# Optimization experiments

Measured on AMD Instinct MI355X. Metric: run time of the kernel, lower is better.

Reference implementation:

```python
import jax, jax.numpy as jnp
import numpy as np

N_SRC = 50000
N_TGT = 50000
E = 320000
D = 256          # feature dim == hidden_channels
H = 256
OUT = 16
L = 2
P_DROP = 0.1
NEG_SLOPE = 0.01  # F.leaky_relu default


def _seg_mean(x, src_idx, dst_idx, n_dst):
    # gather source features along edges, mean-aggregate per destination (PyG SAGE default aggr='mean')
    msgs = x[src_idx]                                            # [E, D]
    s = jax.ops.segment_sum(msgs, dst_idx, num_segments=n_dst)   # [n_dst, D]
    cnt = jax.ops.segment_sum(jnp.ones((dst_idx.shape[0],), x.dtype), dst_idx, num_segments=n_dst)
    return s / jnp.maximum(cnt, 1.0)[:, None]


def _dropout(x, p, key):
    keep = jax.random.bernoulli(key, 1.0 - p, x.shape)
    return jnp.where(keep, x / (1.0 - p), jnp.zeros((), x.dtype))


def setup_inputs() -> dict:
    key = jax.random.key(0)
    ks = jax.random.split(key, 16)
    sc_in = 1.0 / np.sqrt(D)
    sc_h = 1.0 / np.sqrt(H)
    inp = {
        'x_source': jax.random.normal(ks[0], (N_SRC, D), jnp.float32),
        'x_target': jax.random.normal(ks[1], (N_TGT, D), jnp.float32),
        'ei_st': jax.random.randint(ks[2], (2, E), 0, N_SRC, jnp.int32),  # row0: source idx, row1: target idx
        'ei_ts': jax.random.randint(ks[3], (2, E), 0, N_TGT, jnp.int32),  # row0: target idx, row1: source idx
        # SAGEConv params per layer per relation; lin_l has bias, lin_r does not (PyG)
        'Wl_st': jax.random.normal(ks[4], (L, D, H), jnp.float32) * sc_in,
        'Wr_st': jax.random.normal(ks[5], (L, D, H), jnp.float32) * sc_in,
        'b_st': jnp.zeros((L, H), jnp.float32),
        'Wl_ts': jax.random.normal(ks[6], (L, D, H), jnp.float32) * sc_in,
        'Wr_ts': jax.random.normal(ks[7], (L, D, H), jnp.float32) * sc_in,
        'b_ts': jnp.zeros((L, H), jnp.float32),
        'Wout': jax.random.normal(ks[8], (H, OUT), jnp.float32) * sc_h,
        'bout': jnp.zeros((OUT,), jnp.float32),
    }
    return inp


def reference(x_source, x_target, ei_st, ei_ts, Wl_st, Wr_st, b_st, Wl_ts, Wr_ts, b_ts, Wout, bout):
    drop_key = jax.random.key(42)
    x_s, x_t = x_source, x_target
    for l in range(L):
        # relation ('source','edge','target'): messages source -> target
        m_t = _seg_mean(x_s, ei_st[0], ei_st[1], N_TGT)
        new_t = m_t @ Wl_st[l] + b_st[l] + x_t @ Wr_st[l]
        # relation ('target','rev_edge','source'): messages target -> source
        m_s = _seg_mean(x_t, ei_ts[0], ei_ts[1], N_SRC)
        new_s = m_s @ Wl_ts[l] + b_ts[l] + x_s @ Wr_ts[l]
        # leaky_relu + dropout (F.dropout default training=True)
        new_s = jnp.where(new_s >= 0, new_s, NEG_SLOPE * new_s)
        new_t = jnp.where(new_t >= 0, new_t, NEG_SLOPE * new_t)
        x_s = _dropout(new_s, P_DROP, jax.random.fold_in(drop_key, 2 * l))
        x_t = _dropout(new_t, P_DROP, jax.random.fold_in(drop_key, 2 * l + 1))
    return x_s @ Wout + bout  # [N_SRC, OUT]
```

## Files before the change

### kernel.cpp

```cpp
#include <hip/hip_runtime.h>
#include <stdint.h>

#define NSRC 50000
#define NTGT 50000
#define NE   320000
#define DIN  256
#define HID  256
#define DOUT 16

#define GBM 64
#define GBLK ((NSRC + GBM - 1) / GBM)
#define MASK_DW_PER (GBLK * 512)

typedef __attribute__((ext_vector_type(8))) short bf16x8;
typedef __attribute__((ext_vector_type(4))) float f32x4;
typedef __attribute__((ext_vector_type(4))) uint u32x4;

__device__ inline ushort f2b(float f) {
  uint32_t u = __float_as_uint(f);
  return (ushort)((u + 0x7FFFu + ((u >> 16) & 1u)) >> 16);
}
__device__ inline float b2f(ushort h) { return __uint_as_float(((uint32_t)h) << 16); }

typedef __attribute__((address_space(3))) uint32_t lds_u32_t;
typedef const __attribute__((address_space(1))) uint32_t glb_u32_t;
__device__ __forceinline__ void ld_lds16(const ushort* g, ushort* lds) {
  __builtin_amdgcn_global_load_lds((glb_u32_t*)g, (lds_u32_t*)lds, 16, 0, 0);
}

__host__ __device__ constexpr uint64_t tf2x32(uint32_t k0, uint32_t k1,
                                              uint32_t x0, uint32_t x1) {
  uint32_t ks2 = k0 ^ k1 ^ 0x1BD11BDAu;
  x0 += k0; x1 += k1;
#define TF_ROT(x, r) (((x) << (r)) | ((x) >> (32 - (r))))
#define TF_RND(r) { x0 += x1; x1 = TF_ROT(x1, r) ^ x0; }
  TF_RND(13) TF_RND(15) TF_RND(26) TF_RND(6)
  x0 += k1;  x1 += ks2 + 1u;
  TF_RND(17) TF_RND(29) TF_RND(16) TF_RND(24)
  x0 += ks2; x1 += k0 + 2u;
  TF_RND(13) TF_RND(15) TF_RND(26) TF_RND(6)
  x0 += k0;  x1 += k1 + 3u;
  TF_RND(17) TF_RND(29) TF_RND(16) TF_RND(24)
  x0 += k1;  x1 += ks2 + 4u;
  TF_RND(13) TF_RND(15) TF_RND(26) TF_RND(6)
  x0 += ks2; x1 += k0 + 5u;
#undef TF_RND
#undef TF_ROT
  return (uint64_t(x0) << 32) | uint64_t(x1);
}

constexpr uint64_t FOLD[4] = {
  tf2x32(0u, 42u, 0u, 0u),
  tf2x32(0u, 42u, 0u, 1u),
  tf2x32(0u, 42u, 0u, 2u),
  tf2x32(0u, 42u, 0u, 3u),
};

__device__ __forceinline__ void mask_word(uint32_t* __restrict__ masks, int d) {
  int g = d / MASK_DW_PER;
  int w = d - g * MASK_DW_PER;
  int gt = w >> 1, half = w & 1;
  int gblk = gt >> 8, gtid = gt & 255;
  int wave = gtid >> 6, lane = gtid & 63;
  int q = lane >> 4, r = lane & 15;
  uint64_t fk = (g == 0) ? FOLD[1] : (g == 1 ? FOLD[0] : FOLD[2]);
  uint32_t kk0 = (uint32_t)(fk >> 32), kk1 = (uint32_t)fk;
  int mbase = gblk * GBM;
  uint32_t mword = 0;
#pragma unroll
  for (int bb = 0; bb < 32; ++bb) {
    int s = half * 32 + bb;
    int si = s >> 4, se = (s >> 2) & 3, sj = s & 3;
    uint32_t rowg = (uint32_t)(mbase + si * 16 + q * 4 + se);
    uint32_t colg = (uint32_t)(wave * 64 + sj * 16 + r);
    uint64_t rr = tf2x32(kk0, kk1, 0u, rowg * 256u + colg);
    uint32_t bits = (uint32_t)(rr >> 32) ^ (uint32_t)rr;
    mword |= (((bits >> 9) < 7549747u) ? 1u : 0u) << bb;
  }
  masks[d] = mword;
}

#define NB_CVT  25000
#define NB_W    96
#define NB_HIST 2500
#define PREP_T  (NB_CVT + NB_W + NB_HIST)

struct PrepArgs {
  const float *xs, *xt;
  ushort *oxs, *oxt;
  const float* wsrc[6];
  ushort* wdst[6];
  const int *ei_a, *ei_b;
  int *cur_a, *cur_b;
};

__global__ __launch_bounds__(256) void prep_kernel(PrepArgs p) {
  __shared__ ushort tile[64][65];
  int blk = (int)(((long long)blockIdx.x * 97) % PREP_T);
  int tid = threadIdx.x;
  if (blk < NB_CVT) {
    const float* in = blk < (NB_CVT / 2) ? p.xs : p.xt;
    ushort* out = blk < (NB_CVT / 2) ? p.oxs : p.oxt;
    int i = (blk % (NB_CVT / 2)) * 256 + tid;
    float4 v = ((const float4*)in)[i];
    ushort4 o;
    o.x = f2b(v.x); o.y = f2b(v.y); o.z = f2b(v.z); o.w = f2b(v.w);
    ((ushort4*)out)[i] = o;
    return;
  }
  blk -= NB_CVT;
  if (blk < NB_W) {
    const float* W = p.wsrc[blk >> 4];
    ushort* Wt = p.wdst[blk >> 4];
    int ktile = (blk >> 2) & 3, ntile = blk & 3;
#pragma unroll
    for (int rep = 0; rep < 16; ++rep) {
      int lin = rep * 256 + tid;
      int kk = lin >> 6, nn = lin & 63;
      tile[nn][kk] = f2b(W[(size_t)(ktile * 64 + kk) * 256 + ntile * 64 + nn]);
    }
    __syncthreads();
#pragma unroll
    for (int rep = 0; rep < 16; ++rep) {
      int lin = rep * 256 + tid;
      int nn = lin >> 6, kk = lin & 63;
      Wt[(size_t)(ntile * 64 + nn) * 256 + ktile * 64 + kk] = tile[nn][kk];
    }
    return;
  }
  blk -= NB_W;
  const int* ei = blk < (NB_HIST / 2) ? p.ei_a : p.ei_b;
  int* cur = blk < (NB_HIST / 2) ? p.cur_a : p.cur_b;
  int e = (blk % (NB_HIST / 2)) * 256 + tid;
  if (e < NE) atomicAdd(cur + ei[NE + e], 1);
}

#define SB 1024
__global__ __launch_bounds__(SB) void scan_partial(const int* __restrict__ cur_a,
                                                   const int* __restrict__ cur_b,
                                                   int* __restrict__ bsum,
                                                   int n, int nbPer) {
  __shared__ int red[SB];
  int b = blockIdx.x;
  const int* cnt = b < nbPer ? cur_a : cur_b;
  int i = (b % nbPer) * SB + threadIdx.x;
  red[threadIdx.x] = (i < n) ? cnt[i] : 0;
  __syncthreads();
  for (int d = SB / 2; d > 0; d >>= 1) {
    if (threadIdx.x < d) red[threadIdx.x] += red[threadIdx.x + d];
    __syncthreads();
  }
  if (threadIdx.x == 0) bsum[b] = red[0];
}

__global__ __launch_bounds__(128) void scan_base(int* __restrict__ bsum, int nbPer) {
  __shared__ int buf[2][64];
  int half = threadIdx.x >> 6;
  int t = threadIdx.x & 63;
  buf[half][t] = (t < nbPer) ? bsum[half * nbPer + t] : 0;
  __syncthreads();
  for (int d = 1; d < 64; d <<= 1) {
    int v = (t >= d) ? buf[half][t - d] : 0;
    __syncthreads();
    buf[half][t] += v;
    __syncthreads();
  }
  if (t < nbPer) bsum[half * nbPer + t] = (t == 0) ? 0 : buf[half][t - 1];
}

__global__ __launch_bounds__(SB) void scan_final(int* __restrict__ cur_a,
                                                 int* __restrict__ cur_b,
                                                 int* __restrict__ offs_a,
                                                 int* __restrict__ offs_b,
                                                 const int* __restrict__ bsum,
                                                 int n, int nbPer) {
  __shared__ int part[SB];
  int b = blockIdx.x;
  bool first = b < nbPer;
  int* cur = first ? cur_a : cur_b;
  int* offs = first ? offs_a : offs_b;
  int i = (b % nbPer) * SB + threadIdx.x;
  int v = (i < n) ? cur[i] : 0;
  part[threadIdx.x] = v;
  __syncthreads();
  for (int d = 1; d < SB; d <<= 1) {
    int tv = (threadIdx.x >= d) ? part[threadIdx.x - d] : 0;
    __syncthreads();
    part[threadIdx.x] += tv;
    __syncthreads();
  }
  int excl = part[threadIdx.x] - v + bsum[b];
  if (i < n) {
    offs[i] = excl;
    cur[i] = 0;
  }
  if (i == n - 1) offs[n] = excl + v;
}

__global__ __launch_bounds__(256) void csr_fill2(const int* __restrict__ ei_a,
                                                 const int* __restrict__ ei_b,
                                                 const int* __restrict__ offs_a,
                                                 const int* __restrict__ offs_b,
                                                 int* __restrict__ cur_a,
                                                 int* __restrict__ cur_b,
                                                 int* __restrict__ adj_a,
                                                 int* __restrict__ adj_b,
                                                 int nE, int nbPer) {
  int blk = blockIdx.x;
  bool first = blk < nbPer;
  const int* ei = first ? ei_a : ei_b;
  const int* offs = first ? offs_a : offs_b;
  int* cur = first ? cur_a : cur_b;
  int* adj = first ? adj_a : adj_b;
  int e = (blk % nbPer) * 256 + threadIdx.x;
  if (e >= nE) return;
  int dst = ei[nE + e];
  int pos = atomicAdd(cur + dst, 1);
  adj[offs[dst] + pos] = ei[e];
}

#define ACC8(vv)                                                              \
  {                                                                           \
    const ushort* u = (const ushort*)&vv;                                     \
    a0 += b2f(u[0]); a1 += b2f(u[1]); a2 += b2f(u[2]); a3 += b2f(u[3]);       \
    a4 += b2f(u[4]); a5 += b2f(u[5]); a6 += b2f(u[6]); a7 += b2f(u[7]);       \
  }

__device__ __forceinline__ void gather_row8(const ushort* __restrict__ x,
                                            const int* __restrict__ offs,
                                            const int* __restrict__ adj,
                                            ushort* __restrict__ m,
                                            int row, int lane) {
  int start = offs[row], end = offs[row + 1];
  float a0 = 0.f, a1 = 0.f, a2 = 0.f, a3 = 0.f;
  float a4 = 0.f, a5 = 0.f, a6 = 0.f, a7 = 0.f;
  const ushort* xb = x + lane * 8;
  int e = start;
  for (; e + 7 < end; e += 8) {
    int s0 = adj[e],     s1 = adj[e + 1], s2 = adj[e + 2], s3 = adj[e + 3];
    int s4 = adj[e + 4], s5 = adj[e + 5], s6 = adj[e + 6], s7 = adj[e + 7];
    u32x4 v0 = *(const u32x4*)(xb + (size_t)s0 * DIN);
    u32x4 v1 = *(const u32x4*)(xb + (size_t)s1 * DIN);
    u32x4 v2 = *(const u32x4*)(xb + (size_t)s2 * DIN);
    u32x4 v3 = *(const u32x4*)(xb + (size_t)s3 * DIN);
    u32x4 v4 = *(const u32x4*)(xb + (size_t)s4 * DIN);
    u32x4 v5 = *(const u32x4*)(xb + (size_t)s5 * DIN);
    u32x4 v6 = *(const u32x4*)(xb + (size_t)s6 * DIN);
    u32x4 v7 = *(const u32x4*)(xb + (size_t)s7 * DIN);
    ACC8(v0) ACC8(v1) ACC8(v2) ACC8(v3) ACC8(v4) ACC8(v5) ACC8(v6) ACC8(v7)
  }
  for (; e + 3 < end; e += 4) {
    int s0 = adj[e], s1 = adj[e + 1], s2 = adj[e + 2], s3 = adj[e + 3];
    u32x4 v0 = *(const u32x4*)(xb + (size_t)s0 * DIN);
    u32x4 v1 = *(const u32x4*)(xb + (size_t)s1 * DIN);
    u32x4 v2 = *(const u32x4*)(xb + (size_t)s2 * DIN);
    u32x4 v3 = *(const u32x4*)(xb + (size_t)s3 * DIN);
    ACC8(v0) ACC8(v1) ACC8(v2) ACC8(v3)
  }
  for (; e < end; ++e) {
    int s = adj[e];
    u32x4 v = *(const u32x4*)(xb + (size_t)s * DIN);
    ACC8(v)
  }
  float inv = 1.0f / fmaxf((float)(end - start), 1.0f);
  ushort o[8];
  o[0] = f2b(a0 * inv); o[1] = f2b(a1 * inv); o[2] = f2b(a2 * inv); o[3] = f2b(a3 * inv);
  o[4] = f2b(a4 * inv); o[5] = f2b(a5 * inv); o[6] = f2b(a6 * inv); o[7] = f2b(a7 * inv);
  *(u32x4*)(m + (size_t)row * DIN + lane * 8) = *(const u32x4*)o;
}

#define GG_GB 6250
#define G2_MASKB (2 * MASK_DW_PER / 256)
#define GM_T (GG_GB + G2_MASKB)

__global__ __launch_bounds__(256) void gather_mask_h(
    const ushort* __restrict__ x, const int* __restrict__ offs,
    const int* __restrict__ adj, ushort* __restrict__ m,
    uint32_t* __restrict__ masks, int nRows) {
  int blk = (int)(((long long)blockIdx.x * 97) % GM_T);
  int tid = threadIdx.x;
  if (blk >= GG_GB) {
    mask_word(masks, (blk - GG_GB) * 256 + tid);
    return;
  }
  int row = blk * 8 + (tid >> 5);
  if (row < nRows) gather_row8(x, offs, adj, m, row, tid & 31);
}

__device__ __forceinline__ void gemm_kloop(
    int bid, const ushort* __restrict__ A1, const ushort* __restrict__ A2,
    const ushort* __restrict__ W1t, const ushort* __restrict__ W2t,
    int M, ushort* sA, ushort* sB, f32x4 acc[4][4]) {
  const int tid = threadIdx.x;
  const int wave = tid >> 6, lane = tid & 63;
  const int q = lane >> 4, r = lane & 15;
  const int mbase = bid * GBM;

  const int arow = tid >> 2;
  const int akc = (tid & 3) * 8;
  const int agrow = min(mbase + arow, M - 1);
  const ushort* a1p = A1 + (size_t)agrow * DIN + akc;
  const ushort* a2p = A2 + (size_t)agrow * DIN + akc;
  const ushort* w1b = W1t + (size_t)arow * DIN + akc;
  const ushort* w2b = W2t + (size_t)arow * DIN + akc;
  ushort* ldsA0 = sA + wave * 512;
  ushort* ldsA1 = sA + 2048 + wave * 512;

#pragma unroll
  for (int t = 0; t < 8; ++t) {
    const int kt = t * 32;
    __syncthreads();
    ld_lds16(a1p + kt, ldsA0);
    ld_lds16(a2p + kt, ldsA1);
#pragma unroll
    for (int c = 0; c < 4; ++c) {
      ld_lds16(w1b + c * (64 * DIN) + kt, sB + c * 2048 + wave * 512);
      ld_lds16(w2b + c * (64 * DIN) + kt, sB + 8192 + c * 2048 + wave * 512);
    }
    __syncthreads();
#pragma unroll
    for (int ph = 0; ph < 2; ++ph) {
      bf16x8 af[4], bfr[4];
#pragma unroll
      for (int i = 0; i < 4; ++i)
        af[i] = *(const bf16x8*)&sA[ph * 2048 + (i * 16 + r) * 32 + q * 8];
#pragma unroll
      for (int j = 0; j < 4; ++j)
        bfr[j] = *(const bf16x8*)&sB[ph * 8192 + (wave * 64 + j * 16 + r) * 32 + q * 8];
#pragma unroll
      for (int i = 0; i < 4; ++i)
#pragma unroll
        for (int j = 0; j < 4; ++j)
          acc[i][j] = __builtin_amdgcn_mfma_f32_16x16x32_bf16(af[i], bfr[j],
                                                              acc[i][j], 0, 0, 0);
    }
  }
}

__device__ __forceinline__ void gemm_body(
    int bid, const ushort* __restrict__ A1, const ushort* __restrict__ A2,
    const ushort* __restrict__ W1t, const ushort* __restrict__ W2t,
    const float* __restrict__ bias, const uint2* __restrict__ mk,
    ushort* __restrict__ C, int M, ushort* sA, ushort* sB) {
  const int tid = threadIdx.x;
  const int wave = tid >> 6, lane = tid & 63;
  const int q = lane >> 4, r = lane & 15;
  const int mbase = bid * GBM;
  const uint2 km = mk[bid * 256 + tid];

  f32x4 acc[4][4] = {};
  gemm_kloop(bid, A1, A2, W1t, W2t, M, sA, sB, acc);

  float bj[4];
#pragma unroll
  for (int j = 0; j < 4; ++j) bj[j] = bias[wave * 64 + j * 16 + r];
#pragma unroll
  for (int i = 0; i < 4; ++i) {
#pragma unroll
    for (int e = 0; e < 4; ++e) {
      int rowg = mbase + i * 16 + q * 4 + e;
      if (rowg >= M) continue;
#pragma unroll
      for (int j = 0; j < 4; ++j) {
        const int s = i * 16 + e * 4 + j;
        int colg = wave * 64 + j * 16 + r;
        float v = acc[i][j][e] + bj[j];
        v = v >= 0.0f ? v : 0.01f * v;
        uint32_t keep = ((s < 32 ? km.x >> s : km.y >> (s - 32)) & 1u);
        v = keep ? v * (1.0f / 0.9f) : 0.0f;
        C[(size_t)rowg * HID + colg] = f2b(v);
      }
    }
  }
}

__global__ __launch_bounds__(256, 4) void gemm_dual_mfma(
    const ushort* __restrict__ A1, const ushort* __restrict__ A2,
    const ushort* __restrict__ W1t, const ushort* __restrict__ W2t,
    const float* __restrict__ bias, const uint2* __restrict__ mk,
    ushort* __restrict__ C, int M) {
  __shared__ ushort sA[2][GBM * 32];
  __shared__ ushort sB[2][HID * 32];
  gemm_body(blockIdx.x, A1, A2, W1t, W2t, bias, mk, C, M, &sA[0][0], &sB[0][0]);
}

#define GG_MASKB (MASK_DW_PER / 256)
#define G1_T (GBLK + GG_GB + GG_MASKB)

__global__ __launch_bounds__(256, 4) void gemm1_gather(
    const ushort* __restrict__ A1, const ushort* __restrict__ A2,
    const ushort* __restrict__ W1t, const ushort* __restrict__ W2t,
    const float* __restrict__ bias, const uint2* __restrict__ mk,
    ushort* __restrict__ C, int M,
    const ushort* __restrict__ gx, const int* __restrict__ goffs,
    const int* __restrict__ gadj, ushort* __restrict__ gm, int gRows,
    uint32_t* __restrict__ masks) {
  __shared__ ushort sA[2][GBM * 32];
  __shared__ ushort sB[2][HID * 32];
  int blk = (int)(((long long)blockIdx.x * 101) % G1_T);
  if (blk < GBLK) {
    gemm_body(blk, A1, A2, W1t, W2t, bias, mk, C, M, &sA[0][0], &sB[0][0]);
  } else if (blk < GBLK + GG_GB) {
    int row = (blk - GBLK) * 8 + (threadIdx.x >> 5);
    if (row < gRows) gather_row8(gx, goffs, gadj, gm, row, threadIdx.x & 31);
  } else {
    mask_word(masks,
              2 * MASK_DW_PER + (blk - GBLK - GG_GB) * 256 + (int)threadIdx.x);
  }
}

#define GG_T  (GBLK + GG_GB)

__global__ __launch_bounds__(256, 4) void gemm_gather(
    const ushort* __restrict__ A1, const ushort* __restrict__ A2,
    const ushort* __restrict__ W1t, const ushort* __restrict__ W2t,
    const float* __restrict__ bias, const uint2* __restrict__ mk,
    ushort* __restrict__ C, int M,
    const ushort* __restrict__ gx, const int* __restrict__ goffs,
    const int* __restrict__ gadj, ushort* __restrict__ gm, int gRows) {
  __shared__ ushort sA[2][GBM * 32];
  __shared__ ushort sB[2][HID * 32];
  int blk = (int)(((long long)blockIdx.x * 101) % GG_T);
  if (blk < GBLK) {
    gemm_body(blk, A1, A2, W1t, W2t, bias, mk, C, M, &sA[0][0], &sB[0][0]);
  } else {
    int row = (blk - GBLK) * 8 + (threadIdx.x >> 5);
    if (row < gRows) gather_row8(gx, goffs, gadj, gm, row, threadIdx.x & 31);
  }
}

__global__ __launch_bounds__(256) void out_gemm_h(const ushort* __restrict__ X,
                                                  const float* __restrict__ Wout,
                                                  const float* __restrict__ bout,
                                                  float* __restrict__ C, int M) {
  __shared__ float sW[DIN * DOUT];
  int tid = threadIdx.x;
#pragma unroll
  for (int i = 0; i < (DIN * DOUT) / 256; ++i) sW[i * 256 + tid] = Wout[i * 256 + tid];
  __syncthreads();
  int rr = tid >> 4, c = tid & 15;
  int row = blockIdx.x * 16 + rr;
  if (row >= M) return;
  float acc = bout[c];
  const ushort* xp = X + (size_t)row * DIN;
  for (int k = 0; k < DIN; k += 8) {
    uint4 u = *(const uint4*)(xp + k);
    const ushort* us = (const ushort*)&u;
#pragma unroll
    for (int t = 0; t < 8; ++t) acc += b2f(us[t]) * sW[(k + t) * DOUT + c];
  }
  C[(size_t)row * DOUT + c] = acc;
}

extern "C" void kernel_launch(void* const* d_in, const int* in_sizes, int n_in,
                              void* d_out, int out_size, void* d_ws, size_t ws_size,
                              hipStream_t stream) {
  const float* x_source = (const float*)d_in[0];
  const float* x_target = (const float*)d_in[1];
  const int* ei_st = (const int*)d_in[2];
  const int* ei_ts = (const int*)d_in[3];
  const float* Wl_st = (const float*)d_in[4];
  const float* Wr_st = (const float*)d_in[5];
  const float* b_st  = (const float*)d_in[6];
  const float* Wl_ts = (const float*)d_in[7];
  const float* Wr_ts = (const float*)d_in[8];
  const float* b_ts  = (const float*)d_in[9];
  const float* Wout  = (const float*)d_in[10];
  const float* bout  = (const float*)d_in[11];
  float* out = (float*)d_out;

  const size_t F = (size_t)NSRC * DIN;
  const size_t WM = (size_t)DIN * HID;
  const int nbScan = (NSRC + SB - 1) / SB;
  const size_t intCount = (NTGT + 1) + (NSRC + 1) + 2 * NE + NTGT + NSRC +
                          2 * nbScan + 3 * MASK_DW_PER;
  const size_t need = (5 * F + 6 * WM) * sizeof(ushort) + intCount * sizeof(int);
  if (ws_size < need) return;

  ushort* xs0h = (ushort*)d_ws;
  ushort* xt0h = xs0h + F;
  ushort* B0h  = xt0h + F;
  ushort* B1h  = B0h + F;
  ushort* B2h  = B1h + F;
  ushort* wt0  = B2h + F;
  ushort* wt1  = wt0 + WM;
  ushort* wt2  = wt1 + WM;
  ushort* wt3  = wt2 + WM;
  ushort* wt4  = wt3 + WM;
  ushort* wt5  = wt4 + WM;
  int* ip      = (int*)(wt5 + WM);
  int* offs_st = ip;
  int* offs_ts = offs_st + NTGT + 1;
  int* adj_st  = offs_ts + NSRC + 1;
  int* adj_ts  = adj_st + NE;
  int* cur_t   = adj_ts + NE;
  int* cur_s   = cur_t + NTGT;
  int* bsum    = cur_s + NSRC;
  uint32_t* masks = (uint32_t*)(bsum + 2 * nbScan);

  const int EB = (NE + 255) / 256;

  (void)hipMemsetAsync(cur_t, 0, (NTGT + NSRC) * sizeof(int), stream);
  PrepArgs pa;
  pa.xs = x_source; pa.xt = x_target; pa.oxs = xs0h; pa.oxt = xt0h;
  pa.wsrc[0] = Wl_st;      pa.wdst[0] = wt0;
  pa.wsrc[1] = Wr_st;      pa.wdst[1] = wt1;
  pa.wsrc[2] = Wl_ts;      pa.wdst[2] = wt2;
  pa.wsrc[3] = Wr_ts;      pa.wdst[3] = wt3;
  pa.wsrc[4] = Wl_ts + WM; pa.wdst[4] = wt4;
  pa.wsrc[5] = Wr_ts + WM; pa.wdst[5] = wt5;
  pa.ei_a = ei_st; pa.ei_b = ei_ts;
  pa.cur_a = cur_t; pa.cur_b = cur_s;
  prep_kernel<<<PREP_T, 256, 0, stream>>>(pa);

  scan_partial<<<2 * nbScan, SB, 0, stream>>>(cur_t, cur_s, bsum, NTGT, nbScan);
  scan_base<<<1, 128, 0, stream>>>(bsum, nbScan);
  scan_final<<<2 * nbScan, SB, 0, stream>>>(cur_t, cur_s, offs_st, offs_ts,
                                            bsum, NTGT, nbScan);
  csr_fill2<<<2 * EB, 256, 0, stream>>>(ei_st, ei_ts, offs_st, offs_ts,
                                        cur_t, cur_s, adj_st, adj_ts, NE, EB);

  gather_mask_h<<<GM_T, 256, 0, stream>>>(xs0h, offs_st, adj_st, B0h,
                                          masks, NTGT);

  gemm1_gather<<<G1_T, 256, 0, stream>>>(
      B0h, xt0h, wt0, wt1, b_st, (const uint2*)(masks), B2h, NTGT,
      xt0h, offs_ts, adj_ts, B1h, NSRC, masks);

  gemm_gather<<<GG_T, 256, 0, stream>>>(
      B1h, xs0h, wt2, wt3, b_ts, (const uint2*)(masks + MASK_DW_PER), B0h, NSRC,
      B2h, offs_ts, adj_ts, xt0h, NSRC);

  gemm_dual_mfma<<<GBLK, 256, 0, stream>>>(
      xt0h, B0h, wt4, wt5, b_ts + HID, (const uint2*)(masks + 2 * MASK_DW_PER),
      B2h, NSRC);

  out_gemm_h<<<(NSRC + 15) / 16, 256, 0, stream>>>(B2h, Wout, bout, out, NSRC);
}
```

Before: 440.8 us.

## Double-buffer A tiles in LDS and read GEMM weights directly from global

The dual GEMM k-loop no longer stages the transposed weight tiles in shared memory. Each wave now loads its B fragments straight from global memory, relying on the weights staying resident in cache. The activation tiles are double-buffered in LDS, with the next k-slice prefetched while the current one is consumed, so each iteration needs one barrier instead of two. Shared memory per block falls from about 40 KB to 16 KB, which allows higher occupancy. In exchange, the weight loads sit on the critical path without prefetch, and every block re-reads the full weight matrices through the cache.

```diff
diff --git a/kernel.cpp b/kernel.cpp
--- a/kernel.cpp
+++ b/kernel.cpp
@@ -290,7 +290,7 @@
 __device__ __forceinline__ void gemm_kloop(
     int bid, const ushort* __restrict__ A1, const ushort* __restrict__ A2,
     const ushort* __restrict__ W1t, const ushort* __restrict__ W2t,
-    int M, ushort* sA, ushort* sB, f32x4 acc[4][4]) {
+    int M, ushort* sA, f32x4 acc[4][4]) {
   const int tid = threadIdx.x;
   const int wave = tid >> 6, lane = tid & 63;
   const int q = lane >> 4, r = lane & 15;
@@ -301,32 +301,32 @@
   const int agrow = min(mbase + arow, M - 1);
   const ushort* a1p = A1 + (size_t)agrow * DIN + akc;
   const ushort* a2p = A2 + (size_t)agrow * DIN + akc;
-  const ushort* w1b = W1t + (size_t)arow * DIN + akc;
-  const ushort* w2b = W2t + (size_t)arow * DIN + akc;
-  ushort* ldsA0 = sA + wave * 512;
-  ushort* ldsA1 = sA + 2048 + wave * 512;
+  const ushort* w1p = W1t + (size_t)(wave * 64 + r) * DIN + q * 8;
+  const ushort* w2p = W2t + (size_t)(wave * 64 + r) * DIN + q * 8;
+
+  ld_lds16(a1p, sA + wave * 512);
+  ld_lds16(a2p, sA + 2048 + wave * 512);
 
 #pragma unroll
   for (int t = 0; t < 8; ++t) {
     const int kt = t * 32;
     __syncthreads();
-    ld_lds16(a1p + kt, ldsA0);
-    ld_lds16(a2p + kt, ldsA1);
-#pragma unroll
-    for (int c = 0; c < 4; ++c) {
-      ld_lds16(w1b + c * (64 * DIN) + kt, sB + c * 2048 + wave * 512);
-      ld_lds16(w2b + c * (64 * DIN) + kt, sB + 8192 + c * 2048 + wave * 512);
+    if (t < 7) {
+      const int nb = (t + 1) & 1;
+      ld_lds16(a1p + kt + 32, sA + nb * 4096 + wave * 512);
+      ld_lds16(a2p + kt + 32, sA + nb * 4096 + 2048 + wave * 512);
     }
-    __syncthreads();
+    const ushort* sAb = sA + (t & 1) * 4096;
 #pragma unroll
     for (int ph = 0; ph < 2; ++ph) {
+      const ushort* wp = ph ? w2p : w1p;
       bf16x8 af[4], bfr[4];
 #pragma unroll
       for (int i = 0; i < 4; ++i)
-        af[i] = *(const bf16x8*)&sA[ph * 2048 + (i * 16 + r) * 32 + q * 8];
+        af[i] = *(const bf16x8*)&sAb[ph * 2048 + (i * 16 + r) * 32 + q * 8];
 #pragma unroll
       for (int j = 0; j < 4; ++j)
-        bfr[j] = *(const bf16x8*)&sB[ph * 8192 + (wave * 64 + j * 16 + r) * 32 + q * 8];
+        bfr[j] = *(const bf16x8*)(wp + (size_t)(j * 16) * DIN + kt);
 #pragma unroll
       for (int i = 0; i < 4; ++i)
 #pragma unroll
@@ -341,7 +341,7 @@
     int bid, const ushort* __restrict__ A1, const ushort* __restrict__ A2,
     const ushort* __restrict__ W1t, const ushort* __restrict__ W2t,
     const float* __restrict__ bias, const uint2* __restrict__ mk,
-    ushort* __restrict__ C, int M, ushort* sA, ushort* sB) {
+    ushort* __restrict__ C, int M, ushort* sA) {
   const int tid = threadIdx.x;
   const int wave = tid >> 6, lane = tid & 63;
   const int q = lane >> 4, r = lane & 15;
@@ -349,7 +349,7 @@
   const uint2 km = mk[bid * 256 + tid];
 
   f32x4 acc[4][4] = {};
-  gemm_kloop(bid, A1, A2, W1t, W2t, M, sA, sB, acc);
+  gemm_kloop(bid, A1, A2, W1t, W2t, M, sA, acc);
 
   float bj[4];
 #pragma unroll
@@ -379,9 +379,8 @@
     const ushort* __restrict__ W1t, const ushort* __restrict__ W2t,
     const float* __restrict__ bias, const uint2* __restrict__ mk,
     ushort* __restrict__ C, int M) {
-  __shared__ ushort sA[2][GBM * 32];
-  __shared__ ushort sB[2][HID * 32];
-  gemm_body(blockIdx.x, A1, A2, W1t, W2t, bias, mk, C, M, &sA[0][0], &sB[0][0]);
+  __shared__ ushort sA[2][2][GBM * 32];
+  gemm_body(blockIdx.x, A1, A2, W1t, W2t, bias, mk, C, M, &sA[0][0][0]);
 }
 
 #define GG_MASKB (MASK_DW_PER / 256)
@@ -395,11 +394,10 @@
     const ushort* __restrict__ gx, const int* __restrict__ goffs,
     const int* __restrict__ gadj, ushort* __restrict__ gm, int gRows,
     uint32_t* __restrict__ masks) {
-  __shared__ ushort sA[2][GBM * 32];
-  __shared__ ushort sB[2][HID * 32];
+  __shared__ ushort sA[2][2][GBM * 32];
   int blk = (int)(((long long)blockIdx.x * 101) % G1_T);
   if (blk < GBLK) {
-    gemm_body(blk, A1, A2, W1t, W2t, bias, mk, C, M, &sA[0][0], &sB[0][0]);
+    gemm_body(blk, A1, A2, W1t, W2t, bias, mk, C, M, &sA[0][0][0]);
   } else if (blk < GBLK + GG_GB) {
     int row = (blk - GBLK) * 8 + (threadIdx.x >> 5);
     if (row < gRows) gather_row8(gx, goffs, gadj, gm, row, threadIdx.x & 31);
@@ -418,11 +416,10 @@
     ushort* __restrict__ C, int M,
     const ushort* __restrict__ gx, const int* __restrict__ goffs,
     const int* __restrict__ gadj, ushort* __restrict__ gm, int gRows) {
-  __shared__ ushort sA[2][GBM * 32];
-  __shared__ ushort sB[2][HID * 32];
+  __shared__ ushort sA[2][2][GBM * 32];
   int blk = (int)(((long long)blockIdx.x * 101) % GG_T);
   if (blk < GBLK) {
-    gemm_body(blk, A1, A2, W1t, W2t, bias, mk, C, M, &sA[0][0], &sB[0][0]);
+    gemm_body(blk, A1, A2, W1t, W2t, bias, mk, C, M, &sA[0][0][0]);
   } else {
     int row = (blk - GBLK) * 8 + (threadIdx.x >> 5);
     if (row < gRows) gather_row8(gx, goffs, gadj, gm, row, threadIdx.x & 31);
```

New measurement: 477.1 us. 8.2% more time.
